# Optimization experiments

Measured on AMD Instinct MI355X. Metric: run time of the kernel, lower is better.

Reference implementation:

```python
import jax, jax.numpy as jnp
import numpy as np

HEADS = 16
DIM_HEAD = 64
SCALE = DIM_HEAD ** -0.5
EPS = 1e-5


def _bitlinear(x, w):
    """BitNet b1.58 BitLinear (kyegomez/BitNet), eval-mode, bias-free.
    w: [out, in] torch-layout. Ternary weight quant (scale = mean|w|),
    per-token int8 absmax activation quant, straight-through estimator.
    """
    ws = 1.0 / jnp.clip(jnp.mean(jnp.abs(w)), EPS, None)
    wq = jnp.clip(jnp.round(w * ws), -1.0, 1.0) / ws
    wq = w + jax.lax.stop_gradient(wq - w)
    xs = 127.0 / jnp.clip(jnp.max(jnp.abs(x), axis=-1, keepdims=True), EPS, None)
    xq = jnp.clip(jnp.round(x * xs), -128.0, 127.0) / xs
    xq = x + jax.lax.stop_gradient(xq - x)
    return jnp.einsum('bnd,od->bno', xq, wq)


def setup_inputs() -> dict:
    key = jax.random.key(0)
    ks = jax.random.split(key, 6)
    b, n, d = 2, 2048, 1024
    return {
        'x': jax.random.normal(ks[0], (b, n, d), dtype=jnp.float32),
        'context': jax.random.normal(ks[1], (b, n, d), dtype=jnp.float32),
        'Wq': jax.random.normal(ks[2], (d, d), dtype=jnp.float32) * 0.02,
        'Wk': jax.random.normal(ks[3], (d, d), dtype=jnp.float32) * 0.02,
        'Wv': jax.random.normal(ks[4], (d, d), dtype=jnp.float32) * 0.02,
        'Wo': jax.random.normal(ks[5], (d, d), dtype=jnp.float32) * 0.02,
    }


def reference(x, context, Wq, Wk, Wv, Wo):
    b, n, _ = x.shape
    m = context.shape[1]
    q = _bitlinear(x, Wq)
    k = _bitlinear(context, Wk)
    v = _bitlinear(context, Wv)
    # b n (h d) -> b h n d
    q = q.reshape(b, n, HEADS, DIM_HEAD).transpose(0, 2, 1, 3)
    k = k.reshape(b, m, HEADS, DIM_HEAD).transpose(0, 2, 1, 3)
    v = v.reshape(b, m, HEADS, DIM_HEAD).transpose(0, 2, 1, 3)
    dots = jnp.einsum('bhid,bhjd->bhij', q, k) * SCALE
    attn = jax.nn.softmax(dots, axis=-1)  # dropout is identity in eval
    out = jnp.einsum('bhij,bhjd->bhid', attn, v)
    out = out.transpose(0, 2, 1, 3).reshape(b, n, HEADS * DIM_HEAD)
    return _bitlinear(out, Wo)
```

## Files before the change

### kernel.cpp

```cpp
#include <hip/hip_runtime.h>
#include <math.h>

#define HEADS   16
#define DHEAD   64
#define SEQ     2048
#define NB      2
#define DM      1024
#define NTOK    4096
#define WEPS    1e-5

using f16x8   = __attribute__((ext_vector_type(8))) _Float16;
using floatx4 = __attribute__((ext_vector_type(4))) float;
using i32x4   = __attribute__((ext_vector_type(4))) int;

typedef __attribute__((address_space(1))) unsigned int gu32;
typedef __attribute__((address_space(3))) unsigned int lu32;

__device__ __forceinline__ unsigned pack2(_Float16 a, _Float16 b) {
    union { _Float16 h[2]; unsigned u; } c; c.h[0] = a; c.h[1] = b; return c.u;
}
__device__ __forceinline__ _Float16 lo16(unsigned u) {
    union { unsigned u; _Float16 h[2]; } c; c.u = u; return c.h[0];
}
__device__ __forceinline__ _Float16 hi16(unsigned u) {
    union { unsigned u; _Float16 h[2]; } c; c.u = u; return c.h[1];
}

__global__ void wsum1(const float* __restrict__ w0, const float* __restrict__ w1,
                      const float* __restrict__ w2, const float* __restrict__ w3,
                      double* __restrict__ partial) {
    const float* w = (blockIdx.y == 0) ? w0 : (blockIdx.y == 1) ? w1 : (blockIdx.y == 2) ? w2 : w3;
    int base = blockIdx.x * 16384;
    double s = 0.0;
    for (int i = threadIdx.x; i < 16384; i += 256)
        s += fabs((double)w[base + i]);
    __shared__ double sd[256];
    sd[threadIdx.x] = s;
    __syncthreads();
    for (int st = 128; st > 0; st >>= 1) {
        if (threadIdx.x < st) sd[threadIdx.x] += sd[threadIdx.x + st];
        __syncthreads();
    }
    if (threadIdx.x == 0) partial[blockIdx.y * 64 + blockIdx.x] = sd[0];
}

__global__ void wsum2(const double* __restrict__ partial, double* __restrict__ wscale) {
    int t = threadIdx.x;
    if (t < 4) {
        double s = 0.0;
        for (int i = 0; i < 64; i++) s += partial[t * 64 + i];
        double mean = s / (1024.0 * 1024.0);
        wscale[t] = (mean > WEPS) ? mean : WEPS;
    }
}

__global__ void wquant(const float* __restrict__ w0, const float* __restrict__ w1,
                       const float* __restrict__ w2, const float* __restrict__ w3,
                       const double* __restrict__ wscale, signed char* __restrict__ wq) {
    int widx = blockIdx.y;
    const float* w = (widx == 0) ? w0 : (widx == 1) ? w1 : (widx == 2) ? w2 : w3;
    double ws = 1.0 / wscale[widx];
    int idx = (blockIdx.x * 256 + threadIdx.x) * 4;
    float4 wv = *(const float4*)(w + idx);
    char4 o;
    {
        double r = rint((double)wv.x * ws); r = r > 1.0 ? 1.0 : (r < -1.0 ? -1.0 : r); o.x = (signed char)r;
    } {
        double r = rint((double)wv.y * ws); r = r > 1.0 ? 1.0 : (r < -1.0 ? -1.0 : r); o.y = (signed char)r;
    } {
        double r = rint((double)wv.z * ws); r = r > 1.0 ? 1.0 : (r < -1.0 ? -1.0 : r); o.z = (signed char)r;
    } {
        double r = rint((double)wv.w * ws); r = r > 1.0 ? 1.0 : (r < -1.0 ? -1.0 : r); o.w = (signed char)r;
    }
    *(char4*)(wq + (size_t)widx * 1048576 + idx) = o;
}

__device__ __forceinline__ void aquant_row(const float* __restrict__ row,
                                           signed char* __restrict__ dst_row,
                                           double* __restrict__ ascale_p) {
    int t = threadIdx.x;
    float4 xv = *(const float4*)(row + t * 4);
    float a = fmaxf(fmaxf(fabsf(xv.x), fabsf(xv.y)), fmaxf(fabsf(xv.z), fabsf(xv.w)));
    __shared__ float sm[256];
    sm[t] = a;
    __syncthreads();
    for (int st = 128; st > 0; st >>= 1) {
        if (t < st) sm[t] = fmaxf(sm[t], sm[t + st]);
        __syncthreads();
    }
    double mx = (double)sm[0];
    if (mx < WEPS) mx = WEPS;
    if (t == 0) *ascale_p = mx / 127.0;
    double xs = 127.0 / mx;
    char4 o;
    {
        double r = rint((double)xv.x * xs); r = r > 127.0 ? 127.0 : (r < -128.0 ? -128.0 : r); o.x = (signed char)r;
    } {
        double r = rint((double)xv.y * xs); r = r > 127.0 ? 127.0 : (r < -128.0 ? -128.0 : r); o.y = (signed char)r;
    } {
        double r = rint((double)xv.z * xs); r = r > 127.0 ? 127.0 : (r < -128.0 ? -128.0 : r); o.z = (signed char)r;
    } {
        double r = rint((double)xv.w * xs); r = r > 127.0 ? 127.0 : (r < -128.0 ? -128.0 : r); o.w = (signed char)r;
    }
    *(char4*)(dst_row + t * 4) = o;
}

__global__ void aquant(const float* __restrict__ src, signed char* __restrict__ dst,
                       double* __restrict__ ascale) {
    int tok = blockIdx.x;
    aquant_row(src + (size_t)tok * DM, dst + (size_t)tok * DM, ascale + tok);
}

__global__ void aquant2(const float* __restrict__ x, const float* __restrict__ ctx,
                        signed char* __restrict__ dst, double* __restrict__ ascale) {
    int tok = blockIdx.x;
    const float* row = (tok < NTOK) ? x + (size_t)tok * DM : ctx + (size_t)(tok - NTOK) * DM;
    aquant_row(row, dst + (size_t)tok * DM, ascale + tok);
}

__device__ __forceinline__ void gemm_core(
        const signed char* __restrict__ A, const signed char* __restrict__ W,
        const double* __restrict__ ascale, double wsc,
        void* __restrict__ outp, int mode, float prescale, int bx, int by) {
    __shared__ __align__(16) signed char lds_a[128 * 64];
    __shared__ __align__(16) signed char lds_b[128 * 64];
    const int tid  = threadIdx.x;
    const int wave = tid >> 6, lane = tid & 63;
    const int wr = wave >> 1, wc = wave & 1;
    const int quad = lane >> 4, l15 = lane & 15;
    const int row0 = by * 128, col0 = bx * 128;
    i32x4 acc[4][4] = {};

    const signed char* ga0 = A + (size_t)(row0 + (lane >> 2)) * DM + (lane & 3) * 16;
    const signed char* gb0 = W + (size_t)(col0 + (lane >> 2)) * DM + (lane & 3) * 16;

    for (int k0 = 0; k0 < DM; k0 += 64) {
        __syncthreads();
        #pragma unroll
        for (int t = 0; t < 2; t++) {
            const int i = wave + t * 4;
            __builtin_amdgcn_global_load_lds(
                (const gu32*)(const void*)(ga0 + (size_t)i * 16 * DM + k0),
                (lu32*)(void*)(lds_a + i * 1024), 16, 0, 0);
            __builtin_amdgcn_global_load_lds(
                (const gu32*)(const void*)(gb0 + (size_t)i * 16 * DM + k0),
                (lu32*)(void*)(lds_b + i * 1024), 16, 0, 0);
        }
        __syncthreads();
        i32x4 af[4], bfr[4];
        #pragma unroll
        for (int mi = 0; mi < 4; mi++) {
            int r = wr * 64 + mi * 16 + l15;
            af[mi] = *(const i32x4*)&lds_a[r * 64 + quad * 16];
        }
        #pragma unroll
        for (int ni = 0; ni < 4; ni++) {
            int n = wc * 64 + ni * 16 + l15;
            bfr[ni] = *(const i32x4*)&lds_b[n * 64 + quad * 16];
        }
        #pragma unroll
        for (int mi = 0; mi < 4; mi++)
            #pragma unroll
            for (int ni = 0; ni < 4; ni++)
                acc[mi][ni] = __builtin_amdgcn_mfma_i32_16x16x64_i8(af[mi], bfr[ni], acc[mi][ni], 0, 0, 0);
    }

    #pragma unroll
    for (int mi = 0; mi < 4; mi++) {
        int tbase = row0 + wr * 64 + mi * 16 + quad * 4;
        #pragma unroll
        for (int reg = 0; reg < 4; reg++) {
            int t = tbase + reg;
            double sa = ascale[t] * wsc;
            #pragma unroll
            for (int ni = 0; ni < 4; ni++) {
                int o = col0 + wc * 64 + ni * 16 + l15;
                float val = (float)((double)acc[mi][ni][reg] * sa);
                if (mode == 1) {
                    ((float*)outp)[(size_t)t * DM + o] = val;
                } else {
                    int bb = t >> 11, n = t & 2047, hh = o >> 6, dh = o & 63;
                    float fv = val * prescale;
                    _Float16 hl = (_Float16)fv;
                    _Float16 ml = (_Float16)((fv - (float)hl) * 2048.0f);
                    unsigned pw = pack2(hl, ml);
                    if (mode == 0)
                        ((unsigned*)outp)[(((size_t)(bb * HEADS + hh) * SEQ + n) << 6) + dh] = pw;
                    else
                        ((unsigned*)outp)[(((size_t)(bb * HEADS + hh) * 64 + dh) << 11) + n] = pw;
                }
            }
        }
    }
}

__global__ __launch_bounds__(256) void gemm_qkv(
        const signed char* __restrict__ xq, const signed char* __restrict__ cq,
        const signed char* __restrict__ wqb, const double* __restrict__ ascale_x,
        const double* __restrict__ wscale, unsigned* __restrict__ qkv) {
    const int which = blockIdx.x >> 3;
    gemm_core(which == 0 ? xq : cq,
              wqb + (size_t)which * 1048576,
              ascale_x + (which ? NTOK : 0),
              wscale[which],
              qkv + (size_t)which * 4194304,
              which == 2 ? 2 : 0,
              which == 0 ? 0.125f : 1.0f, blockIdx.x & 7, blockIdx.y);
}

__global__ __launch_bounds__(256) void gemm_o(
        const signed char* __restrict__ aq, const signed char* __restrict__ wo,
        const double* __restrict__ ascale, const double* __restrict__ wscale_p,
        float* __restrict__ out) {
    gemm_core(aq, wo, ascale, *wscale_p, out, 1, 1.0f, blockIdx.x, blockIdx.y);
}

#define KH_IDX(row, d8) (((row) * 8 + ((d8) ^ ((row) & 7))) * 8)
#define PP_IDX(row, kc) (((row) * 8 + ((kc) ^ ((row) & 7))) * 4)

__global__ __launch_bounds__(256, 2) void attn_mfma(
        const unsigned* __restrict__ qg, const unsigned* __restrict__ kg,
        const unsigned* __restrict__ vg, float* __restrict__ out) {
    __shared__ __align__(16) _Float16 Kh[32 * 64];
    __shared__ __align__(16) _Float16 Kl[32 * 64];
    __shared__ __align__(16) unsigned Pp[4][32 * 32];
    __shared__ float Lp[4][2][16][4];

    const int bh   = blockIdx.y;
    const int tid  = threadIdx.x;
    const int wave = tid >> 6, lane = tid & 63;
    const int l15  = lane & 15, quad = lane >> 4;
    const int qbase = blockIdx.x * 128 + wave * 32;

    f16x8 qh[2][2], qm[2][2];
    #pragma unroll
    for (int qs = 0; qs < 2; qs++) {
        #pragma unroll
        for (int c = 0; c < 2; c++) {
            const unsigned* qp = qg + (((size_t)bh * SEQ + qbase + qs * 16 + l15) << 6) + c * 32 + quad * 8;
            uint4 a = *(const uint4*)qp;
            uint4 b = *(const uint4*)(qp + 4);
            unsigned wd[8] = {a.x, a.y, a.z, a.w, b.x, b.y, b.z, b.w};
            #pragma unroll
            for (int j = 0; j < 8; j++) {
                qh[qs][c][j] = lo16(wd[j]);
                qm[qs][c][j] = hi16(wd[j]);
            }
        }
    }

    floatx4 och[2][4] = {};
    floatx4 ocm[2][4] = {};
    float lsum[2] = {0.f, 0.f};

    const unsigned* kbase = kg + ((size_t)bh * SEQ << 6);
    const unsigned* vbase = vg + ((size_t)bh << 17);

    for (int kt = 0; kt < SEQ; kt += 32) {
        uint4 va[4], vb[4];
        #pragma unroll
        for (int nh = 0; nh < 4; nh++) {
            const unsigned* vp = vbase + (((size_t)(nh * 16 + l15)) << 11) + kt + quad * 8;
            va[nh] = *(const uint4*)vp;
            vb[nh] = *(const uint4*)(vp + 4);
        }
        __syncthreads();
        {
            int kk = tid >> 3, d8 = tid & 7;
            const unsigned* kp = kbase + (((size_t)(kt + kk)) << 6) + d8 * 8;
            uint4 a = *(const uint4*)kp, b = *(const uint4*)(kp + 4);
            unsigned wd[8] = {a.x, a.y, a.z, a.w, b.x, b.y, b.z, b.w};
            f16x8 hv, lv;
            #pragma unroll
            for (int j = 0; j < 8; j++) { hv[j] = lo16(wd[j]); lv[j] = hi16(wd[j]); }
            *(f16x8*)&Kh[KH_IDX(kk, d8)] = hv;
            *(f16x8*)&Kl[KH_IDX(kk, d8)] = lv;
        }
        __syncthreads();

        f16x8 kfh[2][2], kfl[2][2];
        #pragma unroll
        for (int ms = 0; ms < 2; ms++) {
            #pragma unroll
            for (int c = 0; c < 2; c++) {
                kfh[ms][c] = *(const f16x8*)&Kh[KH_IDX(ms * 16 + l15, c * 4 + quad)];
                kfl[ms][c] = *(const f16x8*)&Kl[KH_IDX(ms * 16 + l15, c * 4 + quad)];
            }
        }

        #pragma unroll
        for (int qs = 0; qs < 2; qs++) {
            #pragma unroll
            for (int ms = 0; ms < 2; ms++) {
                floatx4 ah = {}, am = {};
                #pragma unroll
                for (int c = 0; c < 2; c++) {
                    ah = __builtin_amdgcn_mfma_f32_16x16x32_f16(kfh[ms][c], qh[qs][c], ah, 0, 0, 0);
                    am = __builtin_amdgcn_mfma_f32_16x16x32_f16(kfh[ms][c], qm[qs][c], am, 0, 0, 0);
                    am = __builtin_amdgcn_mfma_f32_16x16x32_f16(kfl[ms][c], qh[qs][c], am, 0, 0, 0);
                }
                float p[4];
                #pragma unroll
                for (int r = 0; r < 4; r++) {
                    float s = ah[r] + am[r] * 4.8828125e-4f;
                    p[r] = __expf(s);
                    lsum[qs] += p[r];
                }
                uint4 w;
                {
                    _Float16 h0 = (_Float16)p[0], m0 = (_Float16)((p[0] - (float)h0) * 2048.0f);
                    _Float16 h1 = (_Float16)p[1], m1 = (_Float16)((p[1] - (float)h1) * 2048.0f);
                    _Float16 h2 = (_Float16)p[2], m2 = (_Float16)((p[2] - (float)h2) * 2048.0f);
                    _Float16 h3 = (_Float16)p[3], m3 = (_Float16)((p[3] - (float)h3) * 2048.0f);
                    w.x = pack2(h0, m0); w.y = pack2(h1, m1);
                    w.z = pack2(h2, m2); w.w = pack2(h3, m3);
                }
                *(uint4*)&Pp[wave][PP_IDX(qs * 16 + l15, ms * 4 + quad)] = w;
            }
        }
        __threadfence_block();

        f16x8 vfh[4], vfm[4];
        #pragma unroll
        for (int nh = 0; nh < 4; nh++) {
            unsigned wd[8] = {va[nh].x, va[nh].y, va[nh].z, va[nh].w,
                              vb[nh].x, vb[nh].y, vb[nh].z, vb[nh].w};
            #pragma unroll
            for (int j = 0; j < 8; j++) { vfh[nh][j] = lo16(wd[j]); vfm[nh][j] = hi16(wd[j]); }
        }
        #pragma unroll
        for (int qs = 0; qs < 2; qs++) {
            uint4 r0 = *(const uint4*)&Pp[wave][PP_IDX(qs * 16 + l15, 2 * quad)];
            uint4 r1 = *(const uint4*)&Pp[wave][PP_IDX(qs * 16 + l15, 2 * quad + 1)];
            unsigned wd[8] = {r0.x, r0.y, r0.z, r0.w, r1.x, r1.y, r1.z, r1.w};
            f16x8 pfh, pfm;
            #pragma unroll
            for (int j = 0; j < 8; j++) { pfh[j] = lo16(wd[j]); pfm[j] = hi16(wd[j]); }
            #pragma unroll
            for (int nh = 0; nh < 4; nh++) {
                och[qs][nh] = __builtin_amdgcn_mfma_f32_16x16x32_f16(pfh, vfh[nh], och[qs][nh], 0, 0, 0);
                ocm[qs][nh] = __builtin_amdgcn_mfma_f32_16x16x32_f16(pfh, vfm[nh], ocm[qs][nh], 0, 0, 0);
                ocm[qs][nh] = __builtin_amdgcn_mfma_f32_16x16x32_f16(pfm, vfh[nh], ocm[qs][nh], 0, 0, 0);
            }
        }
    }

    Lp[wave][0][l15][quad] = lsum[0];
    Lp[wave][1][l15][quad] = lsum[1];
    __threadfence_block();

    int b = bh >> 4, h = bh & 15;
    #pragma unroll
    for (int qs = 0; qs < 2; qs++) {
        float linv[4];
        #pragma unroll
        for (int r = 0; r < 4; r++) {
            float4 lv = *(const float4*)&Lp[wave][qs][quad * 4 + r][0];
            linv[r] = 1.0f / (lv.x + lv.y + lv.z + lv.w);
        }
        #pragma unroll
        for (int nh = 0; nh < 4; nh++) {
            #pragma unroll
            for (int r = 0; r < 4; r++) {
                int token = b * SEQ + qbase + qs * 16 + quad * 4 + r;
                float val = (och[qs][nh][r] + ocm[qs][nh][r] * 4.8828125e-4f) * linv[r];
                out[(size_t)token * DM + h * 64 + nh * 16 + l15] = val;
            }
        }
    }
}

extern "C" void kernel_launch(void* const* d_in, const int* in_sizes, int n_in,
                              void* d_out, int out_size, void* d_ws, size_t ws_size,
                              hipStream_t stream) {
    const float* x       = (const float*)d_in[0];
    const float* context = (const float*)d_in[1];
    const float* Wq      = (const float*)d_in[2];
    const float* Wk      = (const float*)d_in[3];
    const float* Wv      = (const float*)d_in[4];
    const float* Wo      = (const float*)d_in[5];
    char* ws = (char*)d_ws;

    double* wscale   = (double*)(ws + 0);
    double* partial  = (double*)(ws + 4096);
    double* ascale_x = (double*)(ws + 8192);
    double* ascale_a = (double*)(ws + 73728);
    signed char* wqb = (signed char*)(ws + 131072);
    signed char* xq  = (signed char*)(ws + 4325376);
    signed char* cq  = (signed char*)(ws + 8519680);
    float* attn_out  = (float*)(ws + 4325376);
    unsigned* qkvp   = (unsigned*)(ws + 21102592);
    signed char* aq  = (signed char*)(ws + 21102592);

    wsum1<<<dim3(64, 4), 256, 0, stream>>>(Wq, Wk, Wv, Wo, partial);
    wsum2<<<1, 64, 0, stream>>>(partial, wscale);
    wquant<<<dim3(1024, 4), 256, 0, stream>>>(Wq, Wk, Wv, Wo, wscale, wqb);
    aquant2<<<2 * NTOK, 256, 0, stream>>>(x, context, xq, ascale_x);

    gemm_qkv<<<dim3(24, 32), 256, 0, stream>>>(xq, cq, wqb, ascale_x, wscale, qkvp);

    attn_mfma<<<dim3(16, 32), 256, 0, stream>>>(qkvp, qkvp + 4194304, qkvp + 8388608, attn_out);

    aquant<<<NTOK, 256, 0, stream>>>(attn_out, aq, ascale_a);
    gemm_o<<<dim3(8, 32), 256, 0, stream>>>(aq, wqb + 3145728, ascale_a, wscale + 3, (float*)d_out);
}
```

Measured before the change: 315.8 us.

## Split Q/K/P into separate fp16 hi/lo planes and prefetch K tiles

The QKV GEMM now writes Q and K as separate high and low fp16 planes instead of interleaved pairs, so the attention kernel loads MFMA fragments directly without unpacking. K tiles for the next step are prefetched into registers across the loop, and barriers become explicit lgkmcnt waits. The log2(e) factor is folded into the Q prescale so exp2f replaces __expf, and P goes through padded split LDS planes. A linearized grid remaps blocks to heads for locality. Together these cut per-iteration ALU unpacking and global-load latency, at the cost of extra register pressure and more scattered 16-bit stores in the GEMM epilogue.

```diff
diff --git a/kernel.cpp b/kernel.cpp
--- a/kernel.cpp
+++ b/kernel.cpp
@@ -10,12 +10,16 @@
 #define WEPS    1e-5
 
 using f16x8   = __attribute__((ext_vector_type(8))) _Float16;
+using f16x4   = __attribute__((ext_vector_type(4))) _Float16;
 using floatx4 = __attribute__((ext_vector_type(4))) float;
 using i32x4   = __attribute__((ext_vector_type(4))) int;
 
 typedef __attribute__((address_space(1))) unsigned int gu32;
 typedef __attribute__((address_space(3))) unsigned int lu32;
 
+#define BAR_LGKM()  asm volatile("s_waitcnt lgkmcnt(0)\n\ts_barrier" ::: "memory")
+#define WAIT_LGKM() asm volatile("s_waitcnt lgkmcnt(0)" ::: "memory")
+
 __device__ __forceinline__ unsigned pack2(_Float16 a, _Float16 b) {
     union { _Float16 h[2]; unsigned u; } c; c.h[0] = a; c.h[1] = b; return c.u;
 }
@@ -24,6 +28,9 @@
 }
 __device__ __forceinline__ _Float16 hi16(unsigned u) {
     union { unsigned u; _Float16 h[2]; } c; c.u = u; return c.h[1];
+}
+__device__ __forceinline__ unsigned short h16b(_Float16 h) {
+    union { _Float16 h; unsigned short u; } c; c.h = h; return c.u;
 }
 
 __global__ void wsum1(const float* __restrict__ w0, const float* __restrict__ w1,
@@ -183,11 +190,13 @@
                     float fv = val * prescale;
                     _Float16 hl = (_Float16)fv;
                     _Float16 ml = (_Float16)((fv - (float)hl) * 2048.0f);
-                    unsigned pw = pack2(hl, ml);
-                    if (mode == 0)
-                        ((unsigned*)outp)[(((size_t)(bb * HEADS + hh) * SEQ + n) << 6) + dh] = pw;
-                    else
-                        ((unsigned*)outp)[(((size_t)(bb * HEADS + hh) * 64 + dh) << 11) + n] = pw;
+                    if (mode == 0) {
+                        size_t idx = (((size_t)(bb * HEADS + hh) * SEQ + n) << 6) + dh;
+                        ((unsigned short*)outp)[idx]           = h16b(hl);
+                        ((unsigned short*)outp)[idx + 4194304] = h16b(ml);
+                    } else {
+                        ((unsigned*)outp)[(((size_t)(bb * HEADS + hh) * 64 + dh) << 11) + n] = pack2(hl, ml);
+                    }
                 }
             }
         }
@@ -197,15 +206,16 @@
 __global__ __launch_bounds__(256) void gemm_qkv(
         const signed char* __restrict__ xq, const signed char* __restrict__ cq,
         const signed char* __restrict__ wqb, const double* __restrict__ ascale_x,
-        const double* __restrict__ wscale, unsigned* __restrict__ qkv) {
+        const double* __restrict__ wscale, void* __restrict__ qkv) {
     const int which = blockIdx.x >> 3;
+    char* base = (char*)qkv + (size_t)which * 16777216;
     gemm_core(which == 0 ? xq : cq,
               wqb + (size_t)which * 1048576,
               ascale_x + (which ? NTOK : 0),
               wscale[which],
-              qkv + (size_t)which * 4194304,
+              base,
               which == 2 ? 2 : 0,
-              which == 0 ? 0.125f : 1.0f, blockIdx.x & 7, blockIdx.y);
+              which == 0 ? 0.18033688011112042f : 1.0f, blockIdx.x & 7, blockIdx.y);
 }
 
 __global__ __launch_bounds__(256) void gemm_o(
@@ -216,36 +226,33 @@
 }
 
 #define KH_IDX(row, d8) (((row) * 8 + ((d8) ^ ((row) & 7))) * 8)
-#define PP_IDX(row, kc) (((row) * 8 + ((kc) ^ ((row) & 7))) * 4)
 
 __global__ __launch_bounds__(256, 2) void attn_mfma(
-        const unsigned* __restrict__ qg, const unsigned* __restrict__ kg,
+        const unsigned short* __restrict__ qhg, const unsigned short* __restrict__ qlg,
+        const unsigned short* __restrict__ khg, const unsigned short* __restrict__ klg,
         const unsigned* __restrict__ vg, float* __restrict__ out) {
-    __shared__ __align__(16) _Float16 Kh[32 * 64];
-    __shared__ __align__(16) _Float16 Kl[32 * 64];
-    __shared__ __align__(16) unsigned Pp[4][32 * 32];
+    __shared__ __align__(16) _Float16 KhL[32 * 64];
+    __shared__ __align__(16) _Float16 KlL[32 * 64];
+    __shared__ __align__(16) _Float16 PhL[4][32 * 36];
+    __shared__ __align__(16) _Float16 PlL[4][32 * 36];
     __shared__ float Lp[4][2][16][4];
 
-    const int bh   = blockIdx.y;
+    const int lin  = blockIdx.x;
+    const int bh   = (lin & 7) * 4 + (lin >> 7);
+    const int qblk = (lin >> 3) & 15;
     const int tid  = threadIdx.x;
     const int wave = tid >> 6, lane = tid & 63;
     const int l15  = lane & 15, quad = lane >> 4;
-    const int qbase = blockIdx.x * 128 + wave * 32;
+    const int qbase = qblk * 128 + wave * 32;
 
     f16x8 qh[2][2], qm[2][2];
     #pragma unroll
     for (int qs = 0; qs < 2; qs++) {
         #pragma unroll
         for (int c = 0; c < 2; c++) {
-            const unsigned* qp = qg + (((size_t)bh * SEQ + qbase + qs * 16 + l15) << 6) + c * 32 + quad * 8;
-            uint4 a = *(const uint4*)qp;
-            uint4 b = *(const uint4*)(qp + 4);
-            unsigned wd[8] = {a.x, a.y, a.z, a.w, b.x, b.y, b.z, b.w};
-            #pragma unroll
-            for (int j = 0; j < 8; j++) {
-                qh[qs][c][j] = lo16(wd[j]);
-                qm[qs][c][j] = hi16(wd[j]);
-            }
+            size_t off = (((size_t)bh * SEQ + qbase + qs * 16 + l15) << 6) + c * 32 + quad * 8;
+            qh[qs][c] = *(const f16x8*)(qhg + off);
+            qm[qs][c] = *(const f16x8*)(qlg + off);
         }
     }
 
@@ -253,8 +260,14 @@
     floatx4 ocm[2][4] = {};
     float lsum[2] = {0.f, 0.f};
 
-    const unsigned* kbase = kg + ((size_t)bh * SEQ << 6);
+    const unsigned short* khb = khg + ((size_t)bh * SEQ << 6);
+    const unsigned short* klb = klg + ((size_t)bh * SEQ << 6);
     const unsigned* vbase = vg + ((size_t)bh << 17);
+
+    const int kk = tid >> 3, d8 = tid & 7;
+
+    uint4 kh_pf = *(const uint4*)(khb + ((size_t)kk << 6) + d8 * 8);
+    uint4 kl_pf = *(const uint4*)(klb + ((size_t)kk << 6) + d8 * 8);
 
     for (int kt = 0; kt < SEQ; kt += 32) {
         uint4 va[4], vb[4];
@@ -264,27 +277,26 @@
             va[nh] = *(const uint4*)vp;
             vb[nh] = *(const uint4*)(vp + 4);
         }
-        __syncthreads();
-        {
-            int kk = tid >> 3, d8 = tid & 7;
-            const unsigned* kp = kbase + (((size_t)(kt + kk)) << 6) + d8 * 8;
-            uint4 a = *(const uint4*)kp, b = *(const uint4*)(kp + 4);
-            unsigned wd[8] = {a.x, a.y, a.z, a.w, b.x, b.y, b.z, b.w};
-            f16x8 hv, lv;
-            #pragma unroll
-            for (int j = 0; j < 8; j++) { hv[j] = lo16(wd[j]); lv[j] = hi16(wd[j]); }
-            *(f16x8*)&Kh[KH_IDX(kk, d8)] = hv;
-            *(f16x8*)&Kl[KH_IDX(kk, d8)] = lv;
-        }
-        __syncthreads();
+
+        BAR_LGKM();
+
+        *(uint4*)&KhL[KH_IDX(kk, d8)] = kh_pf;
+        *(uint4*)&KlL[KH_IDX(kk, d8)] = kl_pf;
+
+        if (kt + 32 < SEQ) {
+            kh_pf = *(const uint4*)(khb + ((size_t)(kt + 32 + kk) << 6) + d8 * 8);
+            kl_pf = *(const uint4*)(klb + ((size_t)(kt + 32 + kk) << 6) + d8 * 8);
+        }
+
+        BAR_LGKM();
 
         f16x8 kfh[2][2], kfl[2][2];
         #pragma unroll
         for (int ms = 0; ms < 2; ms++) {
             #pragma unroll
             for (int c = 0; c < 2; c++) {
-                kfh[ms][c] = *(const f16x8*)&Kh[KH_IDX(ms * 16 + l15, c * 4 + quad)];
-                kfl[ms][c] = *(const f16x8*)&Kl[KH_IDX(ms * 16 + l15, c * 4 + quad)];
+                kfh[ms][c] = *(const f16x8*)&KhL[KH_IDX(ms * 16 + l15, c * 4 + quad)];
+                kfl[ms][c] = *(const f16x8*)&KlL[KH_IDX(ms * 16 + l15, c * 4 + quad)];
             }
         }
 
@@ -303,22 +315,22 @@
                 #pragma unroll
                 for (int r = 0; r < 4; r++) {
                     float s = ah[r] + am[r] * 4.8828125e-4f;
-                    p[r] = __expf(s);
+                    p[r] = exp2f(s);
                     lsum[qs] += p[r];
                 }
-                uint4 w;
-                {
-                    _Float16 h0 = (_Float16)p[0], m0 = (_Float16)((p[0] - (float)h0) * 2048.0f);
-                    _Float16 h1 = (_Float16)p[1], m1 = (_Float16)((p[1] - (float)h1) * 2048.0f);
-                    _Float16 h2 = (_Float16)p[2], m2 = (_Float16)((p[2] - (float)h2) * 2048.0f);
-                    _Float16 h3 = (_Float16)p[3], m3 = (_Float16)((p[3] - (float)h3) * 2048.0f);
-                    w.x = pack2(h0, m0); w.y = pack2(h1, m1);
-                    w.z = pack2(h2, m2); w.w = pack2(h3, m3);
+                f16x4 hv, lv;
+                #pragma unroll
+                for (int r = 0; r < 4; r++) {
+                    _Float16 h = (_Float16)p[r];
+                    hv[r] = h;
+                    lv[r] = (_Float16)((p[r] - (float)h) * 2048.0f);
                 }
-                *(uint4*)&Pp[wave][PP_IDX(qs * 16 + l15, ms * 4 + quad)] = w;
+                int poff = (qs * 16 + l15) * 36 + ms * 16 + quad * 4;
+                *(f16x4*)&PhL[wave][poff] = hv;
+                *(f16x4*)&PlL[wave][poff] = lv;
             }
         }
-        __threadfence_block();
+        WAIT_LGKM();
 
         f16x8 vfh[4], vfm[4];
         #pragma unroll
@@ -330,12 +342,8 @@
         }
         #pragma unroll
         for (int qs = 0; qs < 2; qs++) {
-            uint4 r0 = *(const uint4*)&Pp[wave][PP_IDX(qs * 16 + l15, 2 * quad)];
-            uint4 r1 = *(const uint4*)&Pp[wave][PP_IDX(qs * 16 + l15, 2 * quad + 1)];
-            unsigned wd[8] = {r0.x, r0.y, r0.z, r0.w, r1.x, r1.y, r1.z, r1.w};
-            f16x8 pfh, pfm;
-            #pragma unroll
-            for (int j = 0; j < 8; j++) { pfh[j] = lo16(wd[j]); pfm[j] = hi16(wd[j]); }
+            f16x8 pfh = *(const f16x8*)&PhL[wave][(qs * 16 + l15) * 36 + quad * 8];
+            f16x8 pfm = *(const f16x8*)&PlL[wave][(qs * 16 + l15) * 36 + quad * 8];
             #pragma unroll
             for (int nh = 0; nh < 4; nh++) {
                 och[qs][nh] = __builtin_amdgcn_mfma_f32_16x16x32_f16(pfh, vfh[nh], och[qs][nh], 0, 0, 0);
@@ -347,7 +355,7 @@
 
     Lp[wave][0][l15][quad] = lsum[0];
     Lp[wave][1][l15][quad] = lsum[1];
-    __threadfence_block();
+    WAIT_LGKM();
 
     int b = bh >> 4, h = bh & 15;
     #pragma unroll
@@ -389,17 +397,23 @@
     signed char* xq  = (signed char*)(ws + 4325376);
     signed char* cq  = (signed char*)(ws + 8519680);
     float* attn_out  = (float*)(ws + 4325376);
-    unsigned* qkvp   = (unsigned*)(ws + 21102592);
+    char* planes     = ws + 21102592;
     signed char* aq  = (signed char*)(ws + 21102592);
+
+    unsigned short* qhg = (unsigned short*)planes;
+    unsigned short* qlg = qhg + 4194304;
+    unsigned short* khg = (unsigned short*)(planes + 16777216);
+    unsigned short* klg = khg + 4194304;
+    unsigned*       vpg = (unsigned*)(planes + 33554432);
 
     wsum1<<<dim3(64, 4), 256, 0, stream>>>(Wq, Wk, Wv, Wo, partial);
     wsum2<<<1, 64, 0, stream>>>(partial, wscale);
     wquant<<<dim3(1024, 4), 256, 0, stream>>>(Wq, Wk, Wv, Wo, wscale, wqb);
     aquant2<<<2 * NTOK, 256, 0, stream>>>(x, context, xq, ascale_x);
 
-    gemm_qkv<<<dim3(24, 32), 256, 0, stream>>>(xq, cq, wqb, ascale_x, wscale, qkvp);
-
-    attn_mfma<<<dim3(16, 32), 256, 0, stream>>>(qkvp, qkvp + 4194304, qkvp + 8388608, attn_out);
+    gemm_qkv<<<dim3(24, 32), 256, 0, stream>>>(xq, cq, wqb, ascale_x, wscale, planes);
+
+    attn_mfma<<<dim3(512), 256, 0, stream>>>(qhg, qlg, khg, klg, vpg, attn_out);
 
     aquant<<<NTOK, 256, 0, stream>>>(attn_out, aq, ascale_a);
     gemm_o<<<dim3(8, 32), 256, 0, stream>>>(aq, wqb + 3145728, ascale_a, wscale + 3, (float*)d_out);
```

Result: faster. 299.0 us (-5.3%).
